# Kernel optimization log

Hardware: AMD Instinct MI355X
Metric: run time of the kernel (lower is better)

Reference implementation:

```python
import jax, jax.numpy as jnp
import numpy as np

B, S, D = 2, 2048, 2048
H, KV = 16, 4
HD = D // H          # 128
QPK = H // KV        # queries per kv head


def setup_inputs() -> dict:
    key = jax.random.key(0)
    ks = jax.random.split(key, 8)
    x = jax.random.normal(ks[0], (B, S, D), jnp.float32)
    mask = jnp.zeros((1, 1, S, S), jnp.float32)  # unused (causal flash path)
    # RoPE tables: theta=10000, shape (S, HD//2)
    inv_freq = 1.0 / (10000.0 ** (jnp.arange(0, HD, 2, dtype=jnp.float32) / HD))
    freqs = jnp.outer(jnp.arange(S, dtype=jnp.float32), inv_freq)
    freqs_cos, freqs_sin = jnp.cos(freqs), jnp.sin(freqs)
    sc = 0.02
    Wq = jax.random.normal(ks[1], (D, H * HD), jnp.float32) * sc
    bq = jnp.zeros((H * HD,), jnp.float32)
    Wk = jax.random.normal(ks[2], (D, KV * HD), jnp.float32) * sc
    bk = jnp.zeros((KV * HD,), jnp.float32)
    Wv = jax.random.normal(ks[3], (D, KV * HD), jnp.float32) * sc
    bv = jnp.zeros((KV * HD,), jnp.float32)
    Wo = jax.random.normal(ks[4], (D, D), jnp.float32) * sc  # bias=False
    return dict(x=x, mask=mask, freqs_cos=freqs_cos, freqs_sin=freqs_sin,
                Wq=Wq, bq=bq, Wk=Wk, bk=bk, Wv=Wv, bv=bv, Wo=Wo)


def _rope(t, cos, sin):
    # t: [B, S, nH, HD]; interleaved-pair rotation as in apply_rope
    tr = t.reshape(t.shape[:-1] + (-1, 2))
    r, i = tr[..., 0], tr[..., 1]
    c = cos[None, :, None, :]
    s = sin[None, :, None, :]
    out = jnp.stack([r * c - i * s, r * s + i * c], axis=-1)
    return out.reshape(t.shape)


def reference(x, mask, freqs_cos, freqs_sin, Wq, bq, Wk, bk, Wv, bv, Wo):
    b, s, d = x.shape
    q = (x @ Wq + bq).reshape(b, s, H, HD)
    k = (x @ Wk + bk).reshape(b, s, KV, HD)
    v = (x @ Wv + bv).reshape(b, s, KV, HD)
    cos, sin = freqs_cos[:s], freqs_sin[:s]
    q = _rope(q, cos, sin)
    k = _rope(k, cos, sin)
    # GQA: repeat_interleave kv heads to match query heads
    k = jnp.repeat(k, QPK, axis=2)
    v = jnp.repeat(v, QPK, axis=2)
    q = q.transpose(0, 2, 1, 3)  # [B, H, S, HD]
    k = k.transpose(0, 2, 1, 3)
    v = v.transpose(0, 2, 1, 3)
    scores = jnp.einsum('bhqd,bhkd->bhqk', q, k) / jnp.sqrt(jnp.float32(HD))
    causal = jnp.tril(jnp.ones((s, s), bool))
    scores = jnp.where(causal[None, None], scores, jnp.finfo(scores.dtype).min)
    attn = jax.nn.softmax(scores, axis=-1)
    out = jnp.einsum('bhqk,bhkd->bhqd', attn, v)
    out = out.transpose(0, 2, 1, 3).reshape(b, s, d)
    return out @ Wo
```

## Files before the change

kernel.cpp:

```cpp
#include <hip/hip_runtime.h>


#define B_  2
#define S_  2048
#define D_  2048
#define H_  16
#define KV_ 4
#define HD_ 128
#define NQK 2560

typedef unsigned short ushort_t;
typedef __attribute__((ext_vector_type(8))) __bf16 bf16x8;
typedef __attribute__((ext_vector_type(4))) float  f32x4;

__device__ __forceinline__ ushort_t f2bf(float f) {
    unsigned u = __float_as_uint(f);
    u += 0x7FFFu + ((u >> 16) & 1u);
    return (ushort_t)(u >> 16);
}
__device__ __forceinline__ float bf2f(ushort_t h) {
    return __uint_as_float(((unsigned)h) << 16);
}

__device__ __forceinline__ void g2l16(const void* g, void* l) {
    __builtin_amdgcn_global_load_lds(
        (const __attribute__((address_space(1))) unsigned int*)g,
        (__attribute__((address_space(3))) unsigned int*)l, 16, 0, 0);
}


__global__ __launch_bounds__(256) void k_prep(
    const float* __restrict__ x,  ushort_t* __restrict__ xb,
    const float* __restrict__ Wq, const float* __restrict__ Wk,
    const float* __restrict__ Wv, const float* __restrict__ Wo,
    ushort_t* __restrict__ Wt, ushort_t* __restrict__ Wot,
    const float* __restrict__ bq, const float* __restrict__ bk,
    const float* __restrict__ bv, float* __restrict__ bb) {
    __shared__ float tile[32][33];
    int id = blockIdx.x, t = threadIdx.x;
    if (id < 8192) {
        int i = id * 256 + t;
        float4 v = ((const float4*)x)[i];
        ushort4 o;
        o.x = f2bf(v.x); o.y = f2bf(v.y); o.z = f2bf(v.z); o.w = f2bf(v.w);
        ((ushort4*)xb)[i] = o;
        return;
    }
    const float* src; ushort_t* dst; int C, bid;
    if (id < 12288)      { src = Wq; dst = Wt;                       C = 2048; bid = id - 8192;  }
    else if (id < 13312) { src = Wk; dst = Wt + (size_t)2048 * 2048; C = 512;  bid = id - 12288; }
    else if (id < 14336) { src = Wv; dst = Wt + (size_t)2560 * 2048; C = 512;  bid = id - 13312; }
    else if (id < 18432) { src = Wo; dst = Wot;                      C = 2048; bid = id - 14336; }
    else {
        int i = (id - 18432) * 256 + t;
        if (i < 3072)
            bb[i] = (i < 2048) ? bq[i] : (i < 2560) ? bk[i - 2048] : bv[i - 2560];
        return;
    }
    const int R = 2048;
    int nbc = C >> 5;
    int c0 = (bid % nbc) * 32, r0 = (bid / nbc) * 32;
    int tx = t & 31, ty = t >> 5;
    for (int i = ty; i < 32; i += 8)
        tile[i][tx] = src[(size_t)(r0 + i) * C + c0 + tx];
    __syncthreads();
    for (int i = ty; i < 32; i += 8)
        dst[(size_t)(c0 + i) * R + r0 + tx] = f2bf(tile[tx][i]);
}


template<int BK>
__global__ __launch_bounds__(256, 3) void k_gemm(const ushort_t* __restrict__ A,
                                                 const ushort_t* __restrict__ Bt,
                                                 void* __restrict__ Cp,
                                                 const float* __restrict__ bias,
                                                 const float* __restrict__ fc,
                                                 const float* __restrict__ fs,
                                                 ushort_t* __restrict__ Vt,
                                                 int M, int N, int K, int out_bf16) {
    constexpr int GPR    = BK / 8;
    constexpr int RPR    = 64 / GPR;
    constexpr int ROUNDS = 32 / RPR;
    __shared__ __align__(16) ushort_t As[128 * BK];
    __shared__ __align__(16) ushort_t Bs[128 * BK];
    int t = threadIdx.x;
    int w = t >> 6, lane = t & 63, quad = lane >> 4, l16 = lane & 15;
    int L = blockIdx.x;
    int mper = (M >> 7) >> 3;
    int xcd = L & 7, j = L >> 3;
    int m0 = (xcd * mper + (j % mper)) * 128;
    int n0 = (j / mper) * 128;
    int wm = (w >> 1) * 64, wn = (w & 1) * 64;
    f32x4 acc[4][4] = {};

    int rlo = lane / GPR;
    int gsl = lane & (GPR - 1);
    const ushort_t* Ag = A  + (size_t)(m0 + w * 32) * K;
    const ushort_t* Bg = Bt + (size_t)(n0 + w * 32) * K;
    int rsw = (l16 & 7);

    for (int k0 = 0; k0 < K; k0 += BK) {
        __syncthreads();
#pragma unroll
        for (int p = 0; p < ROUNDS; p++) {
            int row = p * RPR + rlo;
            int gs = gsl ^ (row & 7);
            g2l16(Ag + (size_t)row * K + k0 + gs * 8, (char*)As + (w * 32 + p * RPR) * 2 * BK);
            g2l16(Bg + (size_t)row * K + k0 + gs * 8, (char*)Bs + (w * 32 + p * RPR) * 2 * BK);
        }
        __syncthreads();
#pragma unroll
        for (int kc = 0; kc < BK / 32; kc++) {
            int gg = quad + kc * 4;
            bf16x8 af[4], bfr[4];
#pragma unroll
            for (int i = 0; i < 4; i++)
                af[i] = *(const bf16x8*)(As + (wm + i * 16 + l16) * BK + ((gg ^ rsw) * 8));
#pragma unroll
            for (int j2 = 0; j2 < 4; j2++)
                bfr[j2] = *(const bf16x8*)(Bs + (wn + j2 * 16 + l16) * BK + ((gg ^ rsw) * 8));
#pragma unroll
            for (int i = 0; i < 4; i++)
#pragma unroll
                for (int j2 = 0; j2 < 4; j2++)
                    acc[i][j2] = __builtin_amdgcn_mfma_f32_16x16x32_bf16(af[i], bfr[j2], acc[i][j2], 0, 0, 0);
        }
    }
    int ostride = fc ? NQK : N;
#pragma unroll
    for (int i = 0; i < 4; i++) {
        int r = m0 + wm + i * 16 + quad * 4;
#pragma unroll
        for (int j2 = 0; j2 < 4; j2++) {
            int c = n0 + wn + j2 * 16 + l16;
            float bv_ = bias ? bias[c] : 0.f;
            if (fc && c >= 2560) {
                ushort4 pack;
                pack.x = f2bf(acc[i][j2][0] + bv_);
                pack.y = f2bf(acc[i][j2][1] + bv_);
                pack.z = f2bf(acc[i][j2][2] + bv_);
                pack.w = f2bf(acc[i][j2][3] + bv_);
                int kv = (c - 2560) >> 7, d = (c - 2560) & 127;
                int b = r >> 11, s0 = r & (S_ - 1);
                *(ushort4*)&Vt[(((size_t)b * KV_ + kv) * HD_ + d) * S_ + s0] = pack;
                continue;
            }
#pragma unroll
            for (int jr = 0; jr < 4; jr++) {
                float v = acc[i][j2][jr] + bv_;
                if (fc) {
                    int s  = (r + jr) & (S_ - 1);
                    int dp = (c & 127) >> 1;
                    float cs = fc[s * 64 + dp], sn = fs[s * 64 + dp];
                    float p = __shfl_xor(v, 1);
                    v = (c & 1) ? (v * cs + p * sn) : (v * cs - p * sn);
                }
                if (out_bf16) ((ushort_t*)Cp)[(size_t)(r + jr) * ostride + c] = f2bf(v);
                else          ((float*)Cp)[(size_t)(r + jr) * ostride + c] = v;
            }
        }
    }
}


#define G1_K  2048
#define G1_NT 32

__global__ __launch_bounds__(512, 2) void k_gemm1_256(
    const ushort_t* __restrict__ A, const ushort_t* __restrict__ Bt,
    ushort_t* __restrict__ C, const float* __restrict__ bias,
    const float* __restrict__ fc, const float* __restrict__ fs,
    ushort_t* __restrict__ Vt) {
    __shared__ __align__(16) ushort_t As[2][16384];
    __shared__ __align__(16) ushort_t Bs[2][16384];
    int t = threadIdx.x;
    int w = t >> 6, lane = t & 63, quad = lane >> 4, l16 = lane & 15;
    int wm_i = w >> 2, wn_i = w & 3;

    int L = blockIdx.x;
    int xcd = L & 7, j = L >> 3;
    int m0 = (xcd * 2 + (j & 1)) * 256;
    int n0 = (j >> 1) * 256;

    int srow = w * 16 + (lane >> 3);
    int sg   = (lane & 7) ^ (lane >> 3);
    const ushort_t* Ag = A  + (size_t)(m0 + srow) * G1_K + sg * 8;
    const ushort_t* Bg = Bt + (size_t)(n0 + srow) * G1_K + sg * 8;

    int swz = l16 & 7;
    int cA = (quad ^ swz) * 8;
    int cB = ((quad + 4) ^ swz) * 8;

    f32x4 acc[8][4] = {};
    bf16x8 afr[4][2], bfr[4][2];

#define ST1A(KT, HA, BUF) do {                                                  \
    const ushort_t* s_ = Ag + (size_t)(HA) * 128 * G1_K + (KT) * 64;            \
    char* d_ = (char*)&As[BUF][(HA) * 8192] + w * 2048;                         \
    g2l16(s_, d_); g2l16(s_ + 8 * G1_K, d_ + 1024); } while (0)
#define ST1B(KT, HB, BUF) do {                                                  \
    const ushort_t* s_ = Bg + (size_t)(HB) * 128 * G1_K + (KT) * 64;            \
    char* d_ = (char*)&Bs[BUF][(HB) * 8192] + w * 2048;                         \
    g2l16(s_, d_); g2l16(s_ + 8 * G1_K, d_ + 1024); } while (0)

#define RDA1(MH, BUF) do {                                                      \
    const ushort_t* Ar = &As[BUF][(wm_i * 128 + (MH) * 64 + l16) * 64];         \
    _Pragma("unroll") for (int ii = 0; ii < 4; ii++) {                          \
        afr[ii][0] = *(const bf16x8*)(Ar + ii * 1024 + cA);                     \
        afr[ii][1] = *(const bf16x8*)(Ar + ii * 1024 + cB); } } while (0)
#define RDB1(NH, BUF) do {                                                      \
    const ushort_t* Br = &Bs[BUF][(wn_i * 64 + (NH) * 32 + l16) * 64];          \
    _Pragma("unroll") for (int jj = 0; jj < 2; jj++) {                          \
        bfr[(NH) * 2 + jj][0] = *(const bf16x8*)(Br + jj * 1024 + cA);          \
        bfr[(NH) * 2 + jj][1] = *(const bf16x8*)(Br + jj * 1024 + cB); } } while (0)

#define MMA1(MH, NH) do {                                                       \
    _Pragma("unroll") for (int kc = 0; kc < 2; kc++)                            \
    _Pragma("unroll") for (int ii = 0; ii < 4; ii++)                            \
    _Pragma("unroll") for (int jj = 0; jj < 2; jj++)                            \
        acc[(MH)*4+ii][(NH)*2+jj] = __builtin_amdgcn_mfma_f32_16x16x32_bf16(    \
            afr[ii][kc], bfr[(NH)*2+jj][kc], acc[(MH)*4+ii][(NH)*2+jj], 0, 0, 0); } while (0)

#define BAR1() __builtin_amdgcn_s_barrier()
#define WGK1() do { asm volatile("s_waitcnt lgkmcnt(0)" ::: "memory");          \
                    __builtin_amdgcn_sched_barrier(0); } while (0)

#define TILE1(KT, BUF, OTH) do {                                                \
             \
    RDA1(0, BUF); RDB1(0, BUF);                                                 \
    if ((KT) + 1 < G1_NT) ST1A((KT) + 1, 0, OTH);                               \
    BAR1(); WGK1();                                                             \
    __builtin_amdgcn_s_setprio(1); MMA1(0, 0); __builtin_amdgcn_s_setprio(0);   \
    BAR1();                                                                     \
                       \
    RDB1(1, BUF);                                                               \
    if ((KT) + 1 < G1_NT) ST1A((KT) + 1, 1, OTH);                               \
    BAR1(); WGK1();                                                             \
    __builtin_amdgcn_s_setprio(1); MMA1(0, 1); __builtin_amdgcn_s_setprio(0);   \
    BAR1();                                                                     \
      \
    RDA1(1, BUF);                                                               \
    if ((KT) + 2 < G1_NT) ST1B((KT) + 2, 0, BUF);                               \
    BAR1(); WGK1();                                                             \
    __builtin_amdgcn_s_setprio(1); MMA1(1, 1); __builtin_amdgcn_s_setprio(0);   \
    BAR1();                                                                     \
         \
    if ((KT) + 2 < G1_NT) ST1B((KT) + 2, 1, BUF);                               \
    if ((KT) < G1_NT - 2) asm volatile("s_waitcnt vmcnt(4)" ::: "memory");      \
    else                  asm volatile("s_waitcnt vmcnt(0)" ::: "memory");      \
    BAR1();                                                                     \
    __builtin_amdgcn_s_setprio(1); MMA1(1, 0); __builtin_amdgcn_s_setprio(0);   \
    BAR1();                                                                     \
} while (0)

    ST1B(0, 0, 0); ST1B(0, 1, 0); ST1A(0, 0, 0); ST1A(0, 1, 0);
    ST1B(1, 0, 1); ST1B(1, 1, 1);
    asm volatile("s_waitcnt vmcnt(4)" ::: "memory");
    BAR1();

    for (int kt = 0; kt < G1_NT; kt += 2) {
        TILE1(kt, 0, 1);
        TILE1(kt + 1, 1, 0);
    }
#undef ST1A
#undef ST1B
#undef RDA1
#undef RDB1
#undef MMA1
#undef BAR1
#undef WGK1
#undef TILE1

#pragma unroll
    for (int i = 0; i < 8; i++) {
        int r = m0 + wm_i * 128 + i * 16 + quad * 4;
#pragma unroll
        for (int j2 = 0; j2 < 4; j2++) {
            int c = n0 + wn_i * 64 + j2 * 16 + l16;
            float bv_ = bias[c];
            if (c >= 2560) {
                ushort4 pack;
                pack.x = f2bf(acc[i][j2][0] + bv_);
                pack.y = f2bf(acc[i][j2][1] + bv_);
                pack.z = f2bf(acc[i][j2][2] + bv_);
                pack.w = f2bf(acc[i][j2][3] + bv_);
                int kv = (c - 2560) >> 7, d = (c - 2560) & 127;
                int b = r >> 11, s0 = r & (S_ - 1);
                *(ushort4*)&Vt[(((size_t)b * KV_ + kv) * HD_ + d) * S_ + s0] = pack;
                continue;
            }
#pragma unroll
            for (int jr = 0; jr < 4; jr++) {
                float v = acc[i][j2][jr] + bv_;
                int s  = (r + jr) & (S_ - 1);
                int dp = (c & 127) >> 1;
                float cs = fc[s * 64 + dp], sn = fs[s * 64 + dp];
                float p = __shfl_xor(v, 1);
                v = (c & 1) ? (v * cs + p * sn) : (v * cs - p * sn);
                C[(size_t)(r + jr) * NQK + c] = f2bf(v);
            }
        }
    }
}


__global__ __launch_bounds__(512, 4) void k_flash(const ushort_t* __restrict__ QK,
                                                  const ushort_t* __restrict__ Vt,
                                                  ushort_t* __restrict__ AO) {
    __shared__ __align__(16) ushort_t Ks[2 * 8192];
    __shared__ __align__(16) ushort_t Vs[2 * 8192];
    __shared__ __align__(16) ushort_t Ps[8 * 16 * 64];
    int h = blockIdx.y, b = blockIdx.z;
    int qt = b ? ((int)gridDim.x - 1 - (int)blockIdx.x) : (int)blockIdx.x;
    int kvh = h >> 2;
    int t = threadIdx.x, w = t >> 6, lane = t & 63, quad = lane >> 4, l16 = lane & 15;
    int qrow0 = qt * 128 + w * 16;
    const float SOFT = 0.08838834764831845f * 1.4426950408889634f;

    bf16x8 aq[4];
    {
        const ushort_t* qb = QK + (size_t)(b * S_ + qrow0 + l16) * NQK + h * HD_ + quad * 8;
#pragma unroll
        for (int kc = 0; kc < 4; kc++) aq[kc] = *(const bf16x8*)(qb + kc * 32);
    }
    bf16x8 vone;
#pragma unroll
    for (int i = 0; i < 8; i++) vone[i] = (__bf16)1.0f;

    f32x4 o[8] = {};
    f32x4 ol = {};
    ushort_t* Psw = Ps + w * 16 * 64;
    int gsw = (l16 >> 1) & 3;

    const ushort_t* kgb = QK + (size_t)(b * S_) * NQK + 2048 + kvh * HD_;
    const ushort_t* vgb = Vt + ((size_t)(b * KV_ + kvh) * HD_) * S_;

    int sr, sgs; char *sK0, *sV0;
    if (t < 256) {
        sr = t >> 2; sgs = (t & 3) ^ ((sr >> 1) & 3);
        sK0 = (char*)Ks + (t >> 6) * 1024;
        sV0 = nullptr;
    } else {
        int u = t - 256;
        sr = u >> 2; sgs = (u & 3) ^ ((sr >> 1) & 3);
        sV0 = (char*)Vs + ((t - 256) >> 6) * 1024;
        sK0 = nullptr;
    }

#define STAGE(KT, BUF)                                                          \
    do {                                                                        \
        if (t < 256) {                                                          \
            const ushort_t* kg = kgb + (size_t)((KT) * 64 + sr) * NQK + sgs * 8; \
            char* KsW = sK0 + (BUF) * 16384;                                    \
            _Pragma("unroll")                                                   \
            for (int p = 0; p < 4; p++) g2l16(kg + p * 32, KsW + p * 4096);     \
        } else {                                                                \
            const ushort_t* vg = vgb + (KT) * 64 + sgs * 8 + (size_t)sr * S_;   \
            char* VsW = sV0 + (BUF) * 16384;                                    \
            _Pragma("unroll")                                                   \
            for (int p = 0; p < 4; p++)                                         \
                g2l16(vg + (size_t)((p & 1) * 64) * S_ + (p >> 1) * 32, VsW + p * 4096); \
        }                                                                       \
    } while (0)

    int ktmax = 2 * qt + 1;
    STAGE(0, 0);
    __syncthreads();

    for (int kt = 0; kt <= ktmax; kt++) {
        int cur = kt & 1;
        if (kt < ktmax) STAGE(kt + 1, cur ^ 1);

        if (kt * 64 <= qrow0 + 15) {
            const ushort_t* Kc = Ks + cur * 8192;
            const ushort_t* Vc = Vs + cur * 8192;
            f32x4 sacc[4] = {};
            __builtin_amdgcn_s_setprio(1);
#pragma unroll
            for (int kc = 0; kc < 4; kc++)
#pragma unroll
                for (int nb = 0; nb < 4; nb++) {
                    bf16x8 bk = *(const bf16x8*)(Kc + kc * 2048 + (nb * 16 + l16) * 32 + ((quad ^ gsw) * 8));
                    sacc[nb] = __builtin_amdgcn_mfma_f32_16x16x32_bf16(aq[kc], bk, sacc[nb], 0, 0, 0);
                }
            __builtin_amdgcn_s_setprio(0);
            if (kt * 64 + 63 > qrow0) {
#pragma unroll
                for (int nb = 0; nb < 4; nb++)
#pragma unroll
                    for (int jr = 0; jr < 4; jr++) {
                        int kcol = kt * 64 + nb * 16 + l16;
                        int qr = qrow0 + quad * 4 + jr;
                        if (kcol > qr) sacc[nb][jr] = -1e30f;
                    }
            }
#pragma unroll
            for (int nb = 0; nb < 4; nb++)
#pragma unroll
                for (int jr = 0; jr < 4; jr++)
                    Psw[(quad * 4 + jr) * 64 + nb * 16 + l16] = f2bf(exp2f(sacc[nb][jr] * SOFT));

            asm volatile("s_waitcnt lgkmcnt(0)" ::: "memory");

            __builtin_amdgcn_s_setprio(1);
#pragma unroll
            for (int kc2 = 0; kc2 < 2; kc2++) {
                bf16x8 ap = *(const bf16x8*)(Psw + l16 * 64 + kc2 * 32 + quad * 8);
                ol = __builtin_amdgcn_mfma_f32_16x16x32_bf16(ap, vone, ol, 0, 0, 0);
#pragma unroll
                for (int db = 0; db < 8; db++) {
                    bf16x8 bv = *(const bf16x8*)(Vc + kc2 * 4096 + (db * 16 + l16) * 32 + ((quad ^ gsw) * 8));
                    o[db] = __builtin_amdgcn_mfma_f32_16x16x32_bf16(ap, bv, o[db], 0, 0, 0);
                }
            }
            __builtin_amdgcn_s_setprio(0);
        }
        __syncthreads();
    }
#undef STAGE

#pragma unroll
    for (int jr = 0; jr < 4; jr++) {
        float inv = 1.0f / ol[jr];
        size_t rbase = (size_t)(b * S_ + qrow0 + quad * 4 + jr) * D_ + h * HD_;
#pragma unroll
        for (int db = 0; db < 8; db++)
            AO[rbase + db * 16 + l16] = f2bf(o[db][jr] * inv);
    }
}


extern "C" void kernel_launch(void* const* d_in, const int* in_sizes, int n_in,
                              void* d_out, int out_size, void* d_ws, size_t ws_size,
                              hipStream_t stream) {
    const float* x  = (const float*)d_in[0];
    const float* fc = (const float*)d_in[2];
    const float* fs = (const float*)d_in[3];
    const float* Wq = (const float*)d_in[4];
    const float* bq = (const float*)d_in[5];
    const float* Wk = (const float*)d_in[6];
    const float* bk = (const float*)d_in[7];
    const float* Wv = (const float*)d_in[8];
    const float* bv = (const float*)d_in[9];
    const float* Wo = (const float*)d_in[10];

    char* ws = (char*)d_ws;
    ushort_t* xb  = (ushort_t*)(ws);
    ushort_t* Wt  = (ushort_t*)(ws + 16777216);
    ushort_t* Wot = (ushort_t*)(ws + 29360128);
    float*    bb  = (float*)   (ws + 37748736);
    ushort_t* QK  = (ushort_t*)(ws + 37761024);
    ushort_t* Vt  = (ushort_t*)(ws + 58732544);
    ushort_t* AO  = xb;
    float* out = (float*)d_out;

    k_prep<<<18444, 256, 0, stream>>>(x, xb, Wq, Wk, Wv, Wo, Wt, Wot, bq, bk, bv, bb);
    k_gemm1_256<<<192, 512, 0, stream>>>(xb, Wt, QK, bb, fc, fs, Vt);
    k_flash<<<dim3(16, 16, 2), 512, 0, stream>>>(QK, Vt, AO);
    k_gemm<128><<<512, 256, 0, stream>>>(AO, Wot, out, nullptr, nullptr, nullptr, nullptr,
                                         4096, 2048, 2048, 0);
}
```

Baseline: 314.8 us.

## Shrink QKV GEMM N-tile to 192 so grid fills all CUs

Changes the fused QKV projection GEMM tile from 256x256 to 256x192, raising the grid from 192 to 256 blocks so every CU gets work. The B-tile staging, LDS buffer size, fragment reads, MMA grouping and vmcnt waits are reorganized for three 64-row B groups. The narrower tile lowers per-block arithmetic intensity and changes the software pipeline balance.

```diff
diff --git a/kernel.cpp b/kernel.cpp
--- a/kernel.cpp
+++ b/kernel.cpp
@@ -172,7 +172,7 @@
     const float* __restrict__ fc, const float* __restrict__ fs,
     ushort_t* __restrict__ Vt) {
     __shared__ __align__(16) ushort_t As[2][16384];
-    __shared__ __align__(16) ushort_t Bs[2][16384];
+    __shared__ __align__(16) ushort_t Bs[2][12288];
     int t = threadIdx.x;
     int w = t >> 6, lane = t & 63, quad = lane >> 4, l16 = lane & 15;
     int wm_i = w >> 2, wn_i = w & 3;
@@ -180,82 +180,84 @@
     int L = blockIdx.x;
     int xcd = L & 7, j = L >> 3;
     int m0 = (xcd * 2 + (j & 1)) * 256;
-    int n0 = (j >> 1) * 256;
+    int n0 = (j >> 1) * 192;
 
     int srow = w * 16 + (lane >> 3);
     int sg   = (lane & 7) ^ (lane >> 3);
-    const ushort_t* Ag = A  + (size_t)(m0 + srow) * G1_K + sg * 8;
-    const ushort_t* Bg = Bt + (size_t)(n0 + srow) * G1_K + sg * 8;
+    const ushort_t* Ag  = A  + (size_t)(m0 + srow) * G1_K + sg * 8;
+    const ushort_t* Bg3 = Bt + (size_t)(n0 + w * 8 + (lane >> 3)) * G1_K + sg * 8;
 
     int swz = l16 & 7;
     int cA = (quad ^ swz) * 8;
     int cB = ((quad + 4) ^ swz) * 8;
 
-    f32x4 acc[8][4] = {};
-    bf16x8 afr[4][2], bfr[4][2];
+    f32x4 acc[8][3] = {};
+    bf16x8 afr[4][2], bfr[3][2];
 
 #define ST1A(KT, HA, BUF) do {                                                  \
     const ushort_t* s_ = Ag + (size_t)(HA) * 128 * G1_K + (KT) * 64;            \
     char* d_ = (char*)&As[BUF][(HA) * 8192] + w * 2048;                         \
     g2l16(s_, d_); g2l16(s_ + 8 * G1_K, d_ + 1024); } while (0)
-#define ST1B(KT, HB, BUF) do {                                                  \
-    const ushort_t* s_ = Bg + (size_t)(HB) * 128 * G1_K + (KT) * 64;            \
-    char* d_ = (char*)&Bs[BUF][(HB) * 8192] + w * 2048;                         \
-    g2l16(s_, d_); g2l16(s_ + 8 * G1_K, d_ + 1024); } while (0)
+#define ST1B(KT, G, BUF) do {                                                   \
+    const ushort_t* s_ = Bg3 + (size_t)(G) * 64 * G1_K + (KT) * 64;             \
+    char* d_ = (char*)&Bs[BUF][(G) * 4096] + w * 1024;                          \
+    g2l16(s_, d_); } while (0)
 
 #define RDA1(MH, BUF) do {                                                      \
     const ushort_t* Ar = &As[BUF][(wm_i * 128 + (MH) * 64 + l16) * 64];         \
     _Pragma("unroll") for (int ii = 0; ii < 4; ii++) {                          \
         afr[ii][0] = *(const bf16x8*)(Ar + ii * 1024 + cA);                     \
         afr[ii][1] = *(const bf16x8*)(Ar + ii * 1024 + cB); } } while (0)
-#define RDB1(NH, BUF) do {                                                      \
-    const ushort_t* Br = &Bs[BUF][(wn_i * 64 + (NH) * 32 + l16) * 64];          \
-    _Pragma("unroll") for (int jj = 0; jj < 2; jj++) {                          \
-        bfr[(NH) * 2 + jj][0] = *(const bf16x8*)(Br + jj * 1024 + cA);          \
-        bfr[(NH) * 2 + jj][1] = *(const bf16x8*)(Br + jj * 1024 + cB); } } while (0)
-
-#define MMA1(MH, NH) do {                                                       \
+#define RDB1(G, BUF) do {                                                       \
+    const ushort_t* Br = &Bs[BUF][(wn_i * 48 + (G) * 16 + l16) * 64];           \
+    bfr[G][0] = *(const bf16x8*)(Br + cA);                                      \
+    bfr[G][1] = *(const bf16x8*)(Br + cB); } while (0)
+
+#define MMA1(MH, G) do {                                                        \
     _Pragma("unroll") for (int kc = 0; kc < 2; kc++)                            \
     _Pragma("unroll") for (int ii = 0; ii < 4; ii++)                            \
-    _Pragma("unroll") for (int jj = 0; jj < 2; jj++)                            \
-        acc[(MH)*4+ii][(NH)*2+jj] = __builtin_amdgcn_mfma_f32_16x16x32_bf16(    \
-            afr[ii][kc], bfr[(NH)*2+jj][kc], acc[(MH)*4+ii][(NH)*2+jj], 0, 0, 0); } while (0)
+        acc[(MH)*4+ii][G] = __builtin_amdgcn_mfma_f32_16x16x32_bf16(            \
+            afr[ii][kc], bfr[G][kc], acc[(MH)*4+ii][G], 0, 0, 0); } while (0)
 
 #define BAR1() __builtin_amdgcn_s_barrier()
 #define WGK1() do { asm volatile("s_waitcnt lgkmcnt(0)" ::: "memory");          \
                     __builtin_amdgcn_sched_barrier(0); } while (0)
 
 #define TILE1(KT, BUF, OTH) do {                                                \
-             \
+                                                                        \
     RDA1(0, BUF); RDB1(0, BUF);                                                 \
     if ((KT) + 1 < G1_NT) ST1A((KT) + 1, 0, OTH);                               \
     BAR1(); WGK1();                                                             \
     __builtin_amdgcn_s_setprio(1); MMA1(0, 0); __builtin_amdgcn_s_setprio(0);   \
     BAR1();                                                                     \
-                       \
-    RDB1(1, BUF);                                                               \
+                                                                        \
+    RDB1(1, BUF); RDB1(2, BUF);                                                 \
     if ((KT) + 1 < G1_NT) ST1A((KT) + 1, 1, OTH);                               \
     BAR1(); WGK1();                                                             \
-    __builtin_amdgcn_s_setprio(1); MMA1(0, 1); __builtin_amdgcn_s_setprio(0);   \
+    __builtin_amdgcn_s_setprio(1); MMA1(0, 1); MMA1(0, 2);                      \
+    __builtin_amdgcn_s_setprio(0);                                              \
     BAR1();                                                                     \
-      \
+          \
     RDA1(1, BUF);                                                               \
-    if ((KT) + 2 < G1_NT) ST1B((KT) + 2, 0, BUF);                               \
+    if ((KT) + 2 < G1_NT) { ST1B((KT) + 2, 0, BUF); ST1B((KT) + 2, 1, BUF); }   \
     BAR1(); WGK1();                                                             \
-    __builtin_amdgcn_s_setprio(1); MMA1(1, 1); __builtin_amdgcn_s_setprio(0);   \
+    __builtin_amdgcn_s_setprio(1); MMA1(1, 2); MMA1(1, 1);                      \
+    __builtin_amdgcn_s_setprio(0);                                              \
     BAR1();                                                                     \
-         \
-    if ((KT) + 2 < G1_NT) ST1B((KT) + 2, 1, BUF);                               \
-    if ((KT) < G1_NT - 2) asm volatile("s_waitcnt vmcnt(4)" ::: "memory");      \
+                              \
+    if ((KT) + 2 < G1_NT) ST1B((KT) + 2, 2, BUF);                               \
+    if ((KT) < G1_NT - 2) asm volatile("s_waitcnt vmcnt(3)" ::: "memory");      \
     else                  asm volatile("s_waitcnt vmcnt(0)" ::: "memory");      \
     BAR1();                                                                     \
+    __builtin_amdgcn_sched_barrier(0);                                          \
     __builtin_amdgcn_s_setprio(1); MMA1(1, 0); __builtin_amdgcn_s_setprio(0);   \
     BAR1();                                                                     \
 } while (0)
 
-    ST1B(0, 0, 0); ST1B(0, 1, 0); ST1A(0, 0, 0); ST1A(0, 1, 0);
-    ST1B(1, 0, 1); ST1B(1, 1, 1);
-    asm volatile("s_waitcnt vmcnt(4)" ::: "memory");
+    ST1B(0, 0, 0); ST1B(0, 1, 0); ST1B(0, 2, 0);
+    ST1A(0, 0, 0); ST1A(0, 1, 0);
+    ST1B(1, 0, 1); ST1B(1, 1, 1); ST1B(1, 2, 1);
+    asm volatile("s_waitcnt vmcnt(3)" ::: "memory");
     BAR1();
 
     for (int kt = 0; kt < G1_NT; kt += 2) {
@@ -275,8 +277,8 @@
     for (int i = 0; i < 8; i++) {
         int r = m0 + wm_i * 128 + i * 16 + quad * 4;
 #pragma unroll
-        for (int j2 = 0; j2 < 4; j2++) {
-            int c = n0 + wn_i * 64 + j2 * 16 + l16;
+        for (int j2 = 0; j2 < 3; j2++) {
+            int c = n0 + wn_i * 48 + j2 * 16 + l16;
             float bv_ = bias[c];
             if (c >= 2560) {
                 ushort4 pack;
@@ -455,7 +457,7 @@
     float* out = (float*)d_out;
 
     k_prep<<<18444, 256, 0, stream>>>(x, xb, Wq, Wk, Wv, Wo, Wt, Wot, bq, bk, bv, bb);
-    k_gemm1_256<<<192, 512, 0, stream>>>(xb, Wt, QK, bb, fc, fs, Vt);
+    k_gemm1_256<<<256, 512, 0, stream>>>(xb, Wt, QK, bb, fc, fs, Vt);
     k_flash<<<dim3(16, 16, 2), 512, 0, stream>>>(QK, Vt, AO);
     k_gemm<128><<<512, 256, 0, stream>>>(AO, Wot, out, nullptr, nullptr, nullptr, nullptr,
                                          4096, 2048, 2048, 0);
```

After: 305.8 us. -2.9%, faster.
